# Kernel optimization log

Measured on AMD Instinct MI355X. Metric: run time of the kernel, lower is better.

## Reference

```python
import jax, jax.numpy as jnp
import numpy as np

N_NODES = 50000
N_EDGES = 800000
D_IN = 128
D_OUT = 128


def setup_inputs() -> dict:
    key = jax.random.key(0)
    k1, k2, k3, k4, k5 = jax.random.split(key, 5)
    x = jax.random.normal(k1, (N_NODES, D_IN), dtype=jnp.float32)
    w = jax.random.normal(k2, (D_IN, D_OUT), dtype=jnp.float32) * (1.0 / np.sqrt(D_IN))
    adj_rows = jnp.sort(jax.random.randint(k3, (N_EDGES,), 0, N_NODES, dtype=jnp.int32))
    adj_cols = jax.random.randint(k4, (N_EDGES,), 0, N_NODES, dtype=jnp.int32)
    adj_vals = jax.random.uniform(k5, (N_EDGES,), dtype=jnp.float32)
    return {"x": x, "w": w, "adj_rows": adj_rows, "adj_cols": adj_cols, "adj_vals": adj_vals}


def reference(x, w, adj_rows, adj_cols, adj_vals):
    # dense feature transform: [N, D_in] @ [D_in, D_out] -> [N, D_out]
    h = jnp.matmul(x, w)
    # sparse adjacency propagation (SpMM in COO form):
    # out[r] = sum over edges (r, c, v) of v * h[c]
    msg = adj_vals[:, None] * h[adj_cols]          # [E, D_out] gather
    out = jax.ops.segment_sum(msg, adj_rows, num_segments=x.shape[0])
    # activation (relu), fused into output pass
    return jax.nn.relu(out)
```

## Files before the change

kernel.cpp:

```cpp
#include <hip/hip_runtime.h>
#include <hip/hip_bf16.h>

#define D 128
#define GEMM_ROWS 32

typedef __bf16 bf16x8 __attribute__((ext_vector_type(8)));
typedef float  f32x4  __attribute__((ext_vector_type(4)));
typedef unsigned int u32x4 __attribute__((ext_vector_type(4)));

__device__ inline bf16x8 cvt_a8(const float* __restrict__ p) {
    float4 v0 = ((const float4*)p)[0], v1 = ((const float4*)p)[1];
    bf16x8 a;
    a[0] = (__bf16)v0.x; a[1] = (__bf16)v0.y; a[2] = (__bf16)v0.z; a[3] = (__bf16)v0.w;
    a[4] = (__bf16)v1.x; a[5] = (__bf16)v1.y; a[6] = (__bf16)v1.z; a[7] = (__bf16)v1.w;
    return a;
}

__global__ __launch_bounds__(256) void fused_gemm_rp(
        const float* __restrict__ x, const float* __restrict__ w,
        const int* __restrict__ rows,
        unsigned short* __restrict__ h, int* __restrict__ rp,
        int n_nodes, int n_edges, int gemm_blocks) {
    const int b = blockIdx.x;

    if (b >= gemm_blocks) {
        int e = (b - gemm_blocks) * 256 + threadIdx.x;
        if (e >= n_edges) return;
        int r    = rows[e];
        int prev = (e == 0) ? -1 : rows[e - 1];
        for (int rr = prev + 1; rr <= r; ++rr) rp[rr] = e;
        if (e == n_edges - 1)
            for (int rr = r + 1; rr <= n_nodes; ++rr) rp[rr] = n_edges;
        return;
    }

    const int wave = threadIdx.x >> 6;
    const int lane = threadIdx.x & 63;
    const int m16  = lane & 15;
    const int q    = lane >> 4;

    const int row0 = b * 64;
    const int col0 = wave * 32;

    bf16x8 bfr[2][4];
#pragma unroll
    for (int t = 0; t < 2; ++t)
#pragma unroll
        for (int s = 0; s < 4; ++s) {
            const float* wp = w + (size_t)(32 * s + q * 8) * D + col0 + 16 * t + m16;
#pragma unroll
            for (int j = 0; j < 8; ++j)
                bfr[t][s][j] = (__bf16)wp[(size_t)j * D];
        }

#pragma unroll 1
    for (int sl = 0; sl < 4; ++sl) {
        const int r = row0 + sl * 16 + m16;
        const float* xp = x + (size_t)r * D + q * 8;

        bf16x8 a[4];
        if (r < n_nodes) {
#pragma unroll
            for (int s = 0; s < 4; ++s) a[s] = cvt_a8(xp + 32 * s);
        } else {
#pragma unroll
            for (int s = 0; s < 4; ++s)
#pragma unroll
                for (int j = 0; j < 8; ++j) a[s][j] = (__bf16)0.f;
        }

        f32x4 acc0 = (f32x4)0.f, acc1 = (f32x4)0.f;
#pragma unroll
        for (int s = 0; s < 4; ++s) {
            acc0 = __builtin_amdgcn_mfma_f32_16x16x32_bf16(a[s], bfr[0][s], acc0, 0, 0, 0);
            acc1 = __builtin_amdgcn_mfma_f32_16x16x32_bf16(a[s], bfr[1][s], acc1, 0, 0, 0);
        }

#pragma unroll
        for (int i = 0; i < 4; ++i) {
            int row = row0 + sl * 16 + q * 4 + i;
            h[(size_t)row * D + col0 + m16]      = __builtin_bit_cast(unsigned short, (__bf16)acc0[i]);
            h[(size_t)row * D + col0 + 16 + m16] = __builtin_bit_cast(unsigned short, (__bf16)acc1[i]);
        }
    }
}

__global__ __launch_bounds__(256) void spmm_bf16_b2(
        const unsigned short* __restrict__ h,
        const int* __restrict__ row_ptr,
        const int* __restrict__ cols,
        const float* __restrict__ vals,
        float* __restrict__ out, int n) {
    const int wave = threadIdx.x >> 6;
    const int lane = threadIdx.x & 63;
    const int r = blockIdx.x * 4 + wave;
    if (r >= n) return;

    const int start = row_ptr[r];
    const int end   = row_ptr[r + 1];
    const int chain = lane >> 4;
    const int l4    = lane & 15;

    const u32x4* h4 = (const u32x4*)h;
    float acc[8];
#pragma unroll
    for (int j = 0; j < 8; ++j) acc[j] = 0.f;

    int e = start + chain;
    int c0 = 0, c1 = 0; float v0 = 0.f, v1 = 0.f;
    if (e < end)     { c0 = cols[e];     v0 = vals[e]; }
    if (e + 4 < end) { c1 = cols[e + 4]; v1 = vals[e + 4]; }

    while (e < end) {
        int en = e + 8;
        int cn0 = 0, cn1 = 0; float vn0 = 0.f, vn1 = 0.f;
        if (en < end)     { cn0 = cols[en];     vn0 = vals[en]; }
        if (en + 4 < end) { cn1 = cols[en + 4]; vn1 = vals[en + 4]; }

        u32x4 hv0 = h4[(size_t)c0 * (D / 8) + l4];
        u32x4 hv1 = h4[(size_t)c1 * (D / 8) + l4];

#pragma unroll
        for (int j = 0; j < 4; ++j) {
            unsigned int u = hv0[j];
            acc[2 * j]     = fmaf(v0, __builtin_bit_cast(float, u << 16),         acc[2 * j]);
            acc[2 * j + 1] = fmaf(v0, __builtin_bit_cast(float, u & 0xFFFF0000u), acc[2 * j + 1]);
        }
#pragma unroll
        for (int j = 0; j < 4; ++j) {
            unsigned int u = hv1[j];
            acc[2 * j]     = fmaf(v1, __builtin_bit_cast(float, u << 16),         acc[2 * j]);
            acc[2 * j + 1] = fmaf(v1, __builtin_bit_cast(float, u & 0xFFFF0000u), acc[2 * j + 1]);
        }
        c0 = cn0; v0 = vn0; c1 = cn1; v1 = vn1; e = en;
    }

#pragma unroll
    for (int j = 0; j < 8; ++j) {
        acc[j] += __shfl_xor(acc[j], 16);
        acc[j] += __shfl_xor(acc[j], 32);
    }

    if (chain == 0) {
        float4 o0, o1;
        o0.x = fmaxf(acc[0], 0.f); o0.y = fmaxf(acc[1], 0.f);
        o0.z = fmaxf(acc[2], 0.f); o0.w = fmaxf(acc[3], 0.f);
        o1.x = fmaxf(acc[4], 0.f); o1.y = fmaxf(acc[5], 0.f);
        o1.z = fmaxf(acc[6], 0.f); o1.w = fmaxf(acc[7], 0.f);
        float4* op = (float4*)(out + (size_t)r * D + l4 * 8);
        op[0] = o0; op[1] = o1;
    }
}

__global__ __launch_bounds__(256) void gemm128(const float* __restrict__ x,
                                               const float* __restrict__ w,
                                               float* __restrict__ h, int n) {
    __shared__ float4 ws4[D * D / 4];
    __shared__ float  xs[GEMM_ROWS][D];
    const int tid  = threadIdx.x;
    const int row0 = blockIdx.x * GEMM_ROWS;
    const float4* w4 = (const float4*)w;
    for (int i = tid; i < D * D / 4; i += 256) ws4[i] = w4[i];
    float4* xs4 = (float4*)&xs[0][0];
    const float4* x4 = (const float4*)x;
    for (int i = tid; i < GEMM_ROWS * D / 4; i += 256) {
        int row = row0 + (i >> 5);
        float4 v = make_float4(0.f, 0.f, 0.f, 0.f);
        if (row < n) v = x4[(size_t)row0 * (D / 4) + i];
        xs4[i] = v;
    }
    __syncthreads();
    const int tx = tid & 31, ty = tid >> 5;
    float4 acc[4];
#pragma unroll
    for (int i = 0; i < 4; ++i) acc[i] = make_float4(0.f, 0.f, 0.f, 0.f);
#pragma unroll 8
    for (int k = 0; k < D; ++k) {
        float4 wv = ws4[k * (D / 4) + tx];
#pragma unroll
        for (int i = 0; i < 4; ++i) {
            float xv = xs[ty * 4 + i][k];
            acc[i].x = fmaf(xv, wv.x, acc[i].x);
            acc[i].y = fmaf(xv, wv.y, acc[i].y);
            acc[i].z = fmaf(xv, wv.z, acc[i].z);
            acc[i].w = fmaf(xv, wv.w, acc[i].w);
        }
    }
#pragma unroll
    for (int i = 0; i < 4; ++i) {
        int row = row0 + ty * 4 + i;
        if (row < n) ((float4*)(h + (size_t)row * D))[tx] = acc[i];
    }
}

__global__ __launch_bounds__(128) void spmm_row(const float* __restrict__ h,
                                                const int* __restrict__ rows,
                                                const int* __restrict__ cols,
                                                const float* __restrict__ vals,
                                                float* __restrict__ out, int n_edges) {
    const int r = blockIdx.x, d = threadIdx.x;
    int lo = 0, hi = n_edges;
    while (lo < hi) { int m = (lo + hi) >> 1; if (rows[m] < r) lo = m + 1; else hi = m; }
    const int start = lo;
    hi = n_edges;
    while (lo < hi) { int m = (lo + hi) >> 1; if (rows[m] <= r) lo = m + 1; else hi = m; }
    const int end = lo;
    float acc = 0.f;
    for (int e = start; e < end; ++e)
        acc = fmaf(vals[e], h[(size_t)cols[e] * D + d], acc);
    out[(size_t)r * D + d] = fmaxf(acc, 0.f);
}

__global__ __launch_bounds__(128) void fused_fallback(
        const float* __restrict__ x, const float* __restrict__ w,
        const int* __restrict__ rows, const int* __restrict__ cols,
        const float* __restrict__ vals, float* __restrict__ out, int n_edges) {
    const int r = blockIdx.x, d = threadIdx.x;
    int lo = 0, hi = n_edges;
    while (lo < hi) { int m = (lo + hi) >> 1; if (rows[m] < r) lo = m + 1; else hi = m; }
    const int start = lo;
    hi = n_edges;
    while (lo < hi) { int m = (lo + hi) >> 1; if (rows[m] <= r) lo = m + 1; else hi = m; }
    const int end = lo;
    float acc = 0.f;
    for (int e = start; e < end; ++e) {
        int c = cols[e]; float v = vals[e];
        float hcd = 0.f;
        for (int k = 0; k < D; ++k)
            hcd = fmaf(x[(size_t)c * D + k], w[(size_t)k * D + d], hcd);
        acc = fmaf(v, hcd, acc);
    }
    out[(size_t)r * D + d] = fmaxf(acc, 0.f);
}

extern "C" void kernel_launch(void* const* d_in, const int* in_sizes, int n_in,
                              void* d_out, int out_size, void* d_ws, size_t ws_size,
                              hipStream_t stream) {
    const float* x    = (const float*)d_in[0];
    const float* w    = (const float*)d_in[1];
    const int*   rows = (const int*)d_in[2];
    const int*   cols = (const int*)d_in[3];
    const float* vals = (const float*)d_in[4];
    float* out = (float*)d_out;

    const int n_nodes = in_sizes[0] / D;
    const int n_edges = in_sizes[2];
    const int n_pad   = (n_nodes + 63) & ~63;

    const size_t h_bytes  = (size_t)n_pad * D * sizeof(unsigned short);
    const size_t rp_off   = h_bytes;
    const size_t need     = rp_off + (size_t)(n_nodes + 1) * sizeof(int);
    const size_t hf_bytes = (size_t)n_nodes * D * sizeof(float);

    if (ws_size >= need) {
        unsigned short* h  = (unsigned short*)d_ws;
        int*            rp = (int*)((char*)d_ws + rp_off);

        const int gemm_blocks = n_pad / 64;
        const int rp_blocks   = (n_edges + 255) / 256;
        fused_gemm_rp<<<gemm_blocks + rp_blocks, 256, 0, stream>>>(
            x, w, rows, h, rp, n_nodes, n_edges, gemm_blocks);

        spmm_bf16_b2<<<(n_nodes + 3) / 4, 256, 0, stream>>>(h, rp, cols, vals, out, n_nodes);
    } else if (ws_size >= hf_bytes) {
        float* hf = (float*)d_ws;
        gemm128<<<(n_nodes + GEMM_ROWS - 1) / GEMM_ROWS, 256, 0, stream>>>(x, w, hf, n_nodes);
        spmm_row<<<n_nodes, 128, 0, stream>>>(hf, rows, cols, vals, out, n_edges);
    } else {
        fused_fallback<<<n_nodes, 128, 0, stream>>>(x, w, rows, cols, vals, out, n_edges);
    }
}
```

Before: 128.4 us.

## Split bf16 h into two column planes and process SpMM per plane

The GEMM now writes h as two separate column planes, each holding 64 of the 128 columns per row, instead of full 128-column rows. The SpMM launches twice as many blocks, and each block handles one plane with 8 lanes per gathered row and 8 edge chains per wave. The aim is a smaller gathered footprint per pass (each plane is half of h) for better cache locality, plus more edges in flight per wave. In exchange, cols, vals and row_ptr are read twice, and the final reduction needs an extra shuffle.

```diff
diff --git a/kernel.cpp b/kernel.cpp
--- a/kernel.cpp
+++ b/kernel.cpp
@@ -20,7 +20,7 @@
         const float* __restrict__ x, const float* __restrict__ w,
         const int* __restrict__ rows,
         unsigned short* __restrict__ h, int* __restrict__ rp,
-        int n_nodes, int n_edges, int gemm_blocks) {
+        int n_nodes, int n_edges, int gemm_blocks, int n_pad) {
     const int b = blockIdx.x;
 
     if (b >= gemm_blocks) {
@@ -53,6 +53,10 @@
                 bfr[t][s][j] = (__bf16)wp[(size_t)j * D];
         }
 
+    const size_t plane_elems = (size_t)n_pad * 64;
+    unsigned short* hp = h + (size_t)(col0 >> 6) * plane_elems;
+    const int pc0 = (col0 & 63) + m16;
+
 #pragma unroll 1
     for (int sl = 0; sl < 4; ++sl) {
         const int r = row0 + sl * 16 + m16;
@@ -79,29 +83,31 @@
 #pragma unroll
         for (int i = 0; i < 4; ++i) {
             int row = row0 + sl * 16 + q * 4 + i;
-            h[(size_t)row * D + col0 + m16]      = __builtin_bit_cast(unsigned short, (__bf16)acc0[i]);
-            h[(size_t)row * D + col0 + 16 + m16] = __builtin_bit_cast(unsigned short, (__bf16)acc1[i]);
-        }
-    }
-}
-
-__global__ __launch_bounds__(256) void spmm_bf16_b2(
+            hp[(size_t)row * 64 + pc0]      = __builtin_bit_cast(unsigned short, (__bf16)acc0[i]);
+            hp[(size_t)row * 64 + pc0 + 16] = __builtin_bit_cast(unsigned short, (__bf16)acc1[i]);
+        }
+    }
+}
+
+__global__ __launch_bounds__(256) void spmm_2plane(
         const unsigned short* __restrict__ h,
         const int* __restrict__ row_ptr,
         const int* __restrict__ cols,
         const float* __restrict__ vals,
-        float* __restrict__ out, int n) {
-    const int wave = threadIdx.x >> 6;
-    const int lane = threadIdx.x & 63;
-    const int r = blockIdx.x * 4 + wave;
+        float* __restrict__ out, int n, int n_pad) {
+    const int plane = blockIdx.x & 1;
+    const int rg    = blockIdx.x >> 1;
+    const int wave  = threadIdx.x >> 6;
+    const int lane  = threadIdx.x & 63;
+    const int r     = rg * 4 + wave;
     if (r >= n) return;
 
     const int start = row_ptr[r];
     const int end   = row_ptr[r + 1];
-    const int chain = lane >> 4;
-    const int l4    = lane & 15;
-
-    const u32x4* h4 = (const u32x4*)h;
+    const int chain = lane >> 3;
+    const int l8    = lane & 7;
+
+    const u32x4* hp = (const u32x4*)(h + (size_t)plane * (size_t)n_pad * 64);
     float acc[8];
 #pragma unroll
     for (int j = 0; j < 8; ++j) acc[j] = 0.f;
@@ -109,16 +115,16 @@
     int e = start + chain;
     int c0 = 0, c1 = 0; float v0 = 0.f, v1 = 0.f;
     if (e < end)     { c0 = cols[e];     v0 = vals[e]; }
-    if (e + 4 < end) { c1 = cols[e + 4]; v1 = vals[e + 4]; }
+    if (e + 8 < end) { c1 = cols[e + 8]; v1 = vals[e + 8]; }
 
     while (e < end) {
-        int en = e + 8;
+        int en = e + 16;
         int cn0 = 0, cn1 = 0; float vn0 = 0.f, vn1 = 0.f;
         if (en < end)     { cn0 = cols[en];     vn0 = vals[en]; }
-        if (en + 4 < end) { cn1 = cols[en + 4]; vn1 = vals[en + 4]; }
-
-        u32x4 hv0 = h4[(size_t)c0 * (D / 8) + l4];
-        u32x4 hv1 = h4[(size_t)c1 * (D / 8) + l4];
+        if (en + 8 < end) { cn1 = cols[en + 8]; vn1 = vals[en + 8]; }
+
+        u32x4 hv0 = hp[(size_t)c0 * 8 + l8];
+        u32x4 hv1 = hp[(size_t)c1 * 8 + l8];
 
 #pragma unroll
         for (int j = 0; j < 4; ++j) {
@@ -137,6 +143,7 @@
 
 #pragma unroll
     for (int j = 0; j < 8; ++j) {
+        acc[j] += __shfl_xor(acc[j], 8);
         acc[j] += __shfl_xor(acc[j], 16);
         acc[j] += __shfl_xor(acc[j], 32);
     }
@@ -147,7 +154,7 @@
         o0.z = fmaxf(acc[2], 0.f); o0.w = fmaxf(acc[3], 0.f);
         o1.x = fmaxf(acc[4], 0.f); o1.y = fmaxf(acc[5], 0.f);
         o1.z = fmaxf(acc[6], 0.f); o1.w = fmaxf(acc[7], 0.f);
-        float4* op = (float4*)(out + (size_t)r * D + l4 * 8);
+        float4* op = (float4*)(out + (size_t)r * D + plane * 64 + l8 * 8);
         op[0] = o0; op[1] = o1;
     }
 }
@@ -259,9 +266,10 @@
         const int gemm_blocks = n_pad / 64;
         const int rp_blocks   = (n_edges + 255) / 256;
         fused_gemm_rp<<<gemm_blocks + rp_blocks, 256, 0, stream>>>(
-            x, w, rows, h, rp, n_nodes, n_edges, gemm_blocks);
-
-        spmm_bf16_b2<<<(n_nodes + 3) / 4, 256, 0, stream>>>(h, rp, cols, vals, out, n_nodes);
+            x, w, rows, h, rp, n_nodes, n_edges, gemm_blocks, n_pad);
+
+        const int rgroups = (n_nodes + 3) / 4;
+        spmm_2plane<<<rgroups * 2, 256, 0, stream>>>(h, rp, cols, vals, out, n_nodes, n_pad);
     } else if (ws_size >= hf_bytes) {
         float* hf = (float*)d_ws;
         gemm128<<<(n_nodes + GEMM_ROWS - 1) / GEMM_ROWS, 256, 0, stream>>>(x, w, hf, n_nodes);
```

New measurement: 133.2 us. 1.04x slower.
